# Performance work log

Hardware: AMD Instinct MI355X
Metric: run time of the kernel (lower is better)

## Reference

```python
import jax, jax.numpy as jnp
import numpy as np
from jax import lax

# minLSTM activation g(x) = x + 0.5 if x >= 0 else sigmoid(x)  (mingru repo functional.g)

def g_act(x):
    return jnp.where(x >= 0, x + 0.5, jax.nn.sigmoid(x))


def conv2d_seq(x5, w, b):
    # x5: (B,S,Cin,H,W), w: (Cout,Cin,3,3), stride 1, pad 1 -> (B,S,Cout,H,W)
    B, S = x5.shape[:2]
    xf = x5.reshape((B * S,) + x5.shape[2:])
    y = lax.conv_general_dilated(xf, w, window_strides=(1, 1),
                                 padding=[(1, 1), (1, 1)],
                                 dimension_numbers=("NCHW", "OIHW", "NCHW"))
    y = y + b[None, :, None, None]
    return y.reshape((B, S) + y.shape[1:])


def minlstm_layer(inp, w, b):
    # inp: (B,S,Cin,H,W) -> out h: (B,S,Cout,H,W)
    gates = conv2d_seq(inp, w, b)                     # (B,S,4C,H,W)
    i_g, f_g, o_g, cand = jnp.split(gates, 4, axis=2)  # each (B,S,C,H,W)
    it = jax.nn.sigmoid(i_g)
    ft = jax.nn.sigmoid(f_g)
    denom = it + ft
    fp = ft / denom                                   # normalized forget gate
    ig = (it / denom) * g_act(cand)                   # normalized input * candidate
    B, S, C, H, W = fp.shape
    # zero-init cell state passes through g: g(0) = 0.5 (init_hidden_state)
    c0 = jnp.full((B, C, H, W), 0.5, dtype=inp.dtype)

    def step(c, xs):
        fpt, igt = xs
        c_new = fpt * c + igt
        return c_new, c_new

    xs = (jnp.moveaxis(fp, 1, 0), jnp.moveaxis(ig, 1, 0))  # (S,B,C,H,W)
    _, cs = lax.scan(step, c0, xs)
    cs = jnp.moveaxis(cs, 0, 1)                       # (B,S,C,H,W)
    h = jax.nn.sigmoid(o_g) * cs                      # output gate
    return h


def setup_inputs() -> dict:
    key = jax.random.key(0)
    ks = jax.random.split(key, 5)
    x = jax.random.normal(ks[0], (4, 16, 32, 32, 32), dtype=jnp.float32)
    w0 = jax.random.normal(ks[1], (256, 32, 3, 3), dtype=jnp.float32) * 0.05
    b0 = jax.random.normal(ks[2], (256,), dtype=jnp.float32) * 0.05
    w1 = jax.random.normal(ks[3], (256, 64, 3, 3), dtype=jnp.float32) * 0.05
    b1 = jax.random.normal(ks[4], (256,), dtype=jnp.float32) * 0.05
    return {"x": x, "w0": w0, "b0": b0, "w1": w1, "b1": b1}


def reference(x, w0, b0, w1, b1):
    out = minlstm_layer(x, w0, b0)
    out = minlstm_layer(out, w1, b1)
    return out  # (B,S,64,H,W) — last layer outputs
```

## Files before the change

### kernel.cpp

```cpp
#include <hip/hip_runtime.h>


typedef __bf16 bf16x8 __attribute__((ext_vector_type(8)));
typedef __bf16 bf16x4 __attribute__((ext_vector_type(4)));
typedef __bf16 bf16x2 __attribute__((ext_vector_type(2)));
typedef float f32x4 __attribute__((ext_vector_type(4)));

#define N_IMG 64
#define HP 34
#define COUT 256

__device__ __forceinline__ float sigf(float x) { return 1.0f / (1.0f + __expf(-x)); }

__device__ __forceinline__ void gload16(void* lds, const void* g) {
  __builtin_amdgcn_global_load_lds(
      (const __attribute__((address_space(1))) void*)g,
      (__attribute__((address_space(3))) void*)lds, 16, 0, 0);
}

__global__ __launch_bounds__(256) void pack_x_k(const float* __restrict__ x,
                                                __bf16* __restrict__ xT) {
  __shared__ float ls[32][33];
  const int n = blockIdx.x >> 5;
  const int h = blockIdx.x & 31;
  const int t = threadIdx.x;
  {
    const int w = t & 31, g4 = t >> 5;
    const float* src = x + (((size_t)n * 32) << 10) + (h << 5);
#pragma unroll
    for (int j = 0; j < 4; ++j) {
      int ci = g4 * 4 + j;
      ls[ci][w] = src[((size_t)ci << 10) + w];
    }
  }
  __syncthreads();
  {
    const int ci = t & 31, w4 = t >> 5;
    __bf16* dst = xT + ((size_t)(n * HP + h + 1) * HP + 1) * 32 + ci;
#pragma unroll
    for (int j = 0; j < 4; ++j) {
      int w = w4 * 4 + j;
      dst[w * 32] = (__bf16)ls[ci][w];
    }
  }
}

template <int CIN>
__global__ __launch_bounds__(256) void pack_w_k(const float* __restrict__ w,
                                                __bf16* __restrict__ wT) {
  int g = blockIdx.x * 256 + threadIdx.x;
  if (g >= 256 * 9 * CIN) return;
  int co = g / (9 * CIN);
  int r = g - co * 9 * CIN;
  int khkw = r / CIN;
  int ci = r - khkw * CIN;
  wT[g] = (__bf16)w[(size_t)(co * CIN + ci) * 9 + khkw];
}

template <int CIN, bool LAYER1>
__global__ __launch_bounds__(256, LAYER1 ? 2 : 4) void conv_gemm_k(
    const __bf16* __restrict__ xT,
    const __bf16* __restrict__ wT,
    const float* __restrict__ bias,
    __bf16* __restrict__ gates) {
  constexpr int NKK = CIN / 32;
  constexpr int CHUNKS = CIN / 8;
  __shared__ bf16x8 lsA[2][CHUNKS * 128];
  __shared__ bf16x8 lsB[2][CHUNKS * 128];

  const int tid = threadIdx.x;
  const int lane = tid & 63;
  const int wid = tid >> 6;
  const int wr = wid >> 1, wc = wid & 1;

  const int bx = blockIdx.x;
  const int by = blockIdx.y;
  const int n = bx >> 3;
  const int h0 = (bx & 7) << 2;
  const int co0 = by << 7;

  f32x4 acc[4][4] = {};
  const size_t wrow = (size_t)9 * CIN;

  auto stage = [&](int buf, int t) {
    const int kh = t / 3;
    const int kw = t - kh * 3;
#pragma unroll
    for (int c = wid; c < 2 * CHUNKS; c += 4) {
      const int chunk = c >> 1;
      const int pix = ((c & 1) << 6) + lane;
      const int hh = h0 + (pix >> 5) + kh;
      const int ww = (pix & 31) + kw;
      gload16((void*)(&lsA[buf][c * 64]),
              (const void*)(xT + ((size_t)(n * HP + hh) * HP + ww) * CIN + chunk * 8));
    }
#pragma unroll
    for (int c = wid; c < 2 * CHUNKS; c += 4) {
      const int chunk = c >> 1;
      const int row = ((c & 1) << 6) + lane;
      gload16((void*)(&lsB[buf][c * 64]),
              (const void*)(wT + (size_t)(co0 + row) * wrow + t * CIN + chunk * 8));
    }
  };

  stage(0, 0);
  __syncthreads();
  int cur = 0;
  for (int t = 0; t < 9; ++t) {
    if (t < 8) stage(cur ^ 1, t + 1);
#pragma unroll
    for (int kk = 0; kk < NKK; ++kk) {
      const int ca = kk * 4 + (lane >> 4);
      bf16x8 af[4], wf[4];
#pragma unroll
      for (int mi = 0; mi < 4; ++mi)
        af[mi] = lsA[cur][ca * 128 + wr * 64 + mi * 16 + (lane & 15)];
#pragma unroll
      for (int ni = 0; ni < 4; ++ni)
        wf[ni] = lsB[cur][ca * 128 + wc * 64 + ni * 16 + (lane & 15)];
#pragma unroll
      for (int mi = 0; mi < 4; ++mi)
#pragma unroll
        for (int ni = 0; ni < 4; ++ni) {
          if constexpr (!LAYER1)
            acc[mi][ni] = __builtin_amdgcn_mfma_f32_16x16x32_bf16(
                af[mi], wf[ni], acc[mi][ni], 0, 0, 0);
          else
            acc[mi][ni] = __builtin_amdgcn_mfma_f32_16x16x32_bf16(
                wf[ni], af[mi], acc[mi][ni], 0, 0, 0);
        }
    }
    __syncthreads();
    cur ^= 1;
  }

#pragma unroll
  for (int mi = 0; mi < 4; ++mi)
#pragma unroll
    for (int ni = 0; ni < 4; ++ni)
#pragma unroll
      for (int r = 0; r < 4; ++r) {
        if constexpr (!LAYER1) {
          const int m_loc = wr * 64 + mi * 16 + ((lane >> 4) << 2) + r;
          const int co = co0 + wc * 64 + ni * 16 + (lane & 15);
          const size_t m = (size_t)bx * 128 + m_loc;
          gates[m * 256 + co] = (__bf16)(acc[mi][ni][r] + bias[co]);
        } else {
          const int co = co0 + wc * 64 + ni * 16 + ((lane >> 4) << 2) + r;
          const int m_loc = wr * 64 + mi * 16 + (lane & 15);
          const int m = bx * 128 + m_loc;
          const int nimg = m >> 10, p = m & 1023;
          gates[((size_t)nimg * 256 + co) * 1024 + p] =
              (__bf16)(acc[mi][ni][r] + bias[co]);
        }
      }
}

__global__ __launch_bounds__(256) void scan0_k(const __bf16* __restrict__ gates,
                                               __bf16* __restrict__ h0T) {
  const int g = blockIdx.x * 256 + threadIdx.x;
  const int c = (g & 31) * 2;
  const int p = (g >> 5) & 1023;
  const int b = g >> 15;
  const int h = p >> 5, w = p & 31;
  float c0 = 0.5f, c1 = 0.5f;
#pragma unroll 4
  for (int s = 0; s < 16; ++s) {
    const size_t base = ((size_t)((b * 16 + s) * 1024 + p)) * 256 + c;
    const bf16x2* gp = reinterpret_cast<const bf16x2*>(gates + base);
    const bf16x2 ig2 = gp[0], fg2 = gp[32], og2 = gp[64], cd2 = gp[96];
    bf16x2 hv2;
#pragma unroll
    for (int j = 0; j < 2; ++j) {
      const float it = sigf((float)ig2[j]), ft = sigf((float)fg2[j]);
      const float inv = 1.0f / (it + ft);
      const float cd_ = (float)cd2[j];
      const float gc = (cd_ >= 0.0f) ? (cd_ + 0.5f) : sigf(cd_);
      float& cst = j ? c1 : c0;
      cst = (ft * inv) * cst + (it * inv) * gc;
      hv2[j] = (__bf16)(sigf((float)og2[j]) * cst);
    }
    *reinterpret_cast<bf16x2*>(
        h0T + ((size_t)((b * 16 + s) * HP + h + 1) * HP + (w + 1)) * 64 + c) = hv2;
  }
}

__global__ __launch_bounds__(256) void scan1_k(const __bf16* __restrict__ gates,
                                               float* __restrict__ out) {
  const int g = blockIdx.x * 256 + threadIdx.x;
  const int p0 = (g & 255) * 4;
  const int c = (g >> 8) & 63;
  const int b = g >> 14;
  float cst[4] = {0.5f, 0.5f, 0.5f, 0.5f};
#pragma unroll 2
  for (int s = 0; s < 16; ++s) {
    const size_t base = ((size_t)(b * 16 + s) * 256 + c) * 1024 + p0;
    const bf16x4 ig4 = *reinterpret_cast<const bf16x4*>(gates + base);
    const bf16x4 fg4 = *reinterpret_cast<const bf16x4*>(gates + base + 64 * 1024);
    const bf16x4 og4 = *reinterpret_cast<const bf16x4*>(gates + base + 128 * 1024);
    const bf16x4 cd4 = *reinterpret_cast<const bf16x4*>(gates + base + 192 * 1024);
    f32x4 hv;
#pragma unroll
    for (int j = 0; j < 4; ++j) {
      const float it = sigf((float)ig4[j]), ft = sigf((float)fg4[j]);
      const float inv = 1.0f / (it + ft);
      const float cd_ = (float)cd4[j];
      const float gc = (cd_ >= 0.0f) ? (cd_ + 0.5f) : sigf(cd_);
      cst[j] = (ft * inv) * cst[j] + (it * inv) * gc;
      hv[j] = sigf((float)og4[j]) * cst[j];
    }
    *reinterpret_cast<f32x4*>(
        out + ((size_t)((b * 16 + s) * 64 + c)) * 1024 + p0) = hv;
  }
}

extern "C" void kernel_launch(void* const* d_in, const int* in_sizes, int n_in,
                              void* d_out, int out_size, void* d_ws,
                              size_t ws_size, hipStream_t stream) {
  const float* x = (const float*)d_in[0];
  const float* w0 = (const float*)d_in[1];
  const float* b0 = (const float*)d_in[2];
  const float* w1 = (const float*)d_in[3];
  const float* b1 = (const float*)d_in[4];
  float* out = (float*)d_out;

  char* ws = (char*)d_ws;
  const size_t XT_BYTES = (size_t)N_IMG * HP * HP * 32 * 2;
  const size_t H0_BYTES = (size_t)N_IMG * HP * HP * 64 * 2;
  const size_t W0T_BYTES = (size_t)256 * 9 * 32 * 2;
  const size_t W1T_BYTES = (size_t)256 * 9 * 64 * 2;
  __bf16* xT = (__bf16*)ws;
  __bf16* h0T = (__bf16*)(ws + XT_BYTES);
  __bf16* w0T = (__bf16*)(ws + XT_BYTES + H0_BYTES);
  __bf16* w1T = (__bf16*)(ws + XT_BYTES + H0_BYTES + W0T_BYTES);
  __bf16* gates = (__bf16*)(ws + XT_BYTES + H0_BYTES + W0T_BYTES + W1T_BYTES);
  (void)ws_size; (void)n_in; (void)in_sizes; (void)out_size;

  hipMemsetAsync(xT, 0, XT_BYTES, stream);
  hipMemsetAsync(h0T, 0, H0_BYTES, stream);

  pack_x_k<<<N_IMG * 32, 256, 0, stream>>>(x, xT);
  pack_w_k<32><<<(256 * 9 * 32 + 255) / 256, 256, 0, stream>>>(w0, w0T);
  pack_w_k<64><<<(256 * 9 * 64 + 255) / 256, 256, 0, stream>>>(w1, w1T);

  conv_gemm_k<32, false><<<dim3(512, 2), 256, 0, stream>>>(xT, w0T, b0, gates);
  scan0_k<<<512, 256, 0, stream>>>(gates, h0T);
  conv_gemm_k<64, true><<<dim3(512, 2), 256, 0, stream>>>(h0T, w1T, b1, gates);
  scan1_k<<<256, 256, 0, stream>>>(gates, out);
}
```

Baseline: 188.6 us.

## Load input halo plane once into LDS and index taps from it

The conv GEMM now loads a 6x34 padded input plane per block into LDS once, instead of re-staging a shifted im2col tile for every one of the nine taps. A-fragments are read at per-tap offsets, so only the weight tile stays double-buffered per tap. This is meant to cut redundant global loads of activations. It uses synchronous vector loads for the plane, adds LDS bank-conflict risk from the 34-wide stride, and changes layer-0 occupancy to 2. Separately, scan0 processes 4 channels per thread with half the blocks.

```diff
diff --git a/kernel.cpp b/kernel.cpp
--- a/kernel.cpp
+++ b/kernel.cpp
@@ -58,20 +58,23 @@
 }
 
 template <int CIN, bool LAYER1>
-__global__ __launch_bounds__(256, LAYER1 ? 2 : 4) void conv_gemm_k(
+__global__ __launch_bounds__(256, 2) void conv_gemm_k(
     const __bf16* __restrict__ xT,
     const __bf16* __restrict__ wT,
     const float* __restrict__ bias,
     __bf16* __restrict__ gates) {
   constexpr int NKK = CIN / 32;
   constexpr int CHUNKS = CIN / 8;
-  __shared__ bf16x8 lsA[2][CHUNKS * 128];
+  constexpr int PLANE = 204;
+  __shared__ bf16x8 lsA[CHUNKS * PLANE];
   __shared__ bf16x8 lsB[2][CHUNKS * 128];
 
   const int tid = threadIdx.x;
   const int lane = tid & 63;
   const int wid = tid >> 6;
   const int wr = wid >> 1, wc = wid & 1;
+  const int g = lane >> 4;
+  const int li = lane & 15;
 
   const int bx = blockIdx.x;
   const int by = blockIdx.y;
@@ -82,18 +85,23 @@
   f32x4 acc[4][4] = {};
   const size_t wrow = (size_t)9 * CIN;
 
-  auto stage = [&](int buf, int t) {
-    const int kh = t / 3;
-    const int kw = t - kh * 3;
-#pragma unroll
-    for (int c = wid; c < 2 * CHUNKS; c += 4) {
-      const int chunk = c >> 1;
-      const int pix = ((c & 1) << 6) + lane;
-      const int hh = h0 + (pix >> 5) + kh;
-      const int ww = (pix & 31) + kw;
-      gload16((void*)(&lsA[buf][c * 64]),
-              (const void*)(xT + ((size_t)(n * HP + hh) * HP + ww) * CIN + chunk * 8));
-    }
+  for (int gi = tid; gi < CHUNKS * PLANE; gi += 256) {
+    const int ch = gi & (CHUNKS - 1);
+    const int pos = gi / CHUNKS;
+    const int r = pos / 34;
+    const int w = pos - r * 34;
+    lsA[ch * PLANE + pos] = *reinterpret_cast<const bf16x8*>(
+        xT + ((size_t)(n * HP + h0 + r) * HP + w) * CIN + ch * 8);
+  }
+
+  int posm[4];
+#pragma unroll
+  for (int mi = 0; mi < 4; ++mi) {
+    const int m = wr * 64 + mi * 16 + li;
+    posm[mi] = (m >> 5) * 34 + (m & 31);
+  }
+
+  auto stageB = [&](int buf, int t) {
 #pragma unroll
     for (int c = wid; c < 2 * CHUNKS; c += 4) {
       const int chunk = c >> 1;
@@ -103,21 +111,25 @@
     }
   };
 
-  stage(0, 0);
+  stageB(0, 0);
   __syncthreads();
   int cur = 0;
+#pragma unroll
   for (int t = 0; t < 9; ++t) {
-    if (t < 8) stage(cur ^ 1, t + 1);
+    const int kh = t / 3;
+    const int kw = t - kh * 3;
+    const int tapoff = kh * 34 + kw;
+    if (t < 8) stageB(cur ^ 1, t + 1);
 #pragma unroll
     for (int kk = 0; kk < NKK; ++kk) {
-      const int ca = kk * 4 + (lane >> 4);
+      const int ca = kk * 4 + g;
       bf16x8 af[4], wf[4];
 #pragma unroll
       for (int mi = 0; mi < 4; ++mi)
-        af[mi] = lsA[cur][ca * 128 + wr * 64 + mi * 16 + (lane & 15)];
+        af[mi] = lsA[ca * PLANE + posm[mi] + tapoff];
 #pragma unroll
       for (int ni = 0; ni < 4; ++ni)
-        wf[ni] = lsB[cur][ca * 128 + wc * 64 + ni * 16 + (lane & 15)];
+        wf[ni] = lsB[cur][ca * 128 + wc * 64 + ni * 16 + li];
 #pragma unroll
       for (int mi = 0; mi < 4; ++mi)
 #pragma unroll
@@ -141,13 +153,13 @@
 #pragma unroll
       for (int r = 0; r < 4; ++r) {
         if constexpr (!LAYER1) {
-          const int m_loc = wr * 64 + mi * 16 + ((lane >> 4) << 2) + r;
-          const int co = co0 + wc * 64 + ni * 16 + (lane & 15);
+          const int m_loc = wr * 64 + mi * 16 + (g << 2) + r;
+          const int co = co0 + wc * 64 + ni * 16 + li;
           const size_t m = (size_t)bx * 128 + m_loc;
           gates[m * 256 + co] = (__bf16)(acc[mi][ni][r] + bias[co]);
         } else {
-          const int co = co0 + wc * 64 + ni * 16 + ((lane >> 4) << 2) + r;
-          const int m_loc = wr * 64 + mi * 16 + (lane & 15);
+          const int co = co0 + wc * 64 + ni * 16 + (g << 2) + r;
+          const int m_loc = wr * 64 + mi * 16 + li;
           const int m = bx * 128 + m_loc;
           const int nimg = m >> 10, p = m & 1023;
           gates[((size_t)nimg * 256 + co) * 1024 + p] =
@@ -159,29 +171,28 @@
 __global__ __launch_bounds__(256) void scan0_k(const __bf16* __restrict__ gates,
                                                __bf16* __restrict__ h0T) {
   const int g = blockIdx.x * 256 + threadIdx.x;
-  const int c = (g & 31) * 2;
-  const int p = (g >> 5) & 1023;
-  const int b = g >> 15;
+  const int c = (g & 15) * 4;
+  const int p = (g >> 4) & 1023;
+  const int b = g >> 14;
   const int h = p >> 5, w = p & 31;
-  float c0 = 0.5f, c1 = 0.5f;
+  float cst[4] = {0.5f, 0.5f, 0.5f, 0.5f};
 #pragma unroll 4
   for (int s = 0; s < 16; ++s) {
     const size_t base = ((size_t)((b * 16 + s) * 1024 + p)) * 256 + c;
-    const bf16x2* gp = reinterpret_cast<const bf16x2*>(gates + base);
-    const bf16x2 ig2 = gp[0], fg2 = gp[32], og2 = gp[64], cd2 = gp[96];
-    bf16x2 hv2;
-#pragma unroll
-    for (int j = 0; j < 2; ++j) {
-      const float it = sigf((float)ig2[j]), ft = sigf((float)fg2[j]);
+    const bf16x4* gp = reinterpret_cast<const bf16x4*>(gates + base);
+    const bf16x4 ig4 = gp[0], fg4 = gp[16], og4 = gp[32], cd4 = gp[48];
+    bf16x4 hv4;
+#pragma unroll
+    for (int j = 0; j < 4; ++j) {
+      const float it = sigf((float)ig4[j]), ft = sigf((float)fg4[j]);
       const float inv = 1.0f / (it + ft);
-      const float cd_ = (float)cd2[j];
+      const float cd_ = (float)cd4[j];
       const float gc = (cd_ >= 0.0f) ? (cd_ + 0.5f) : sigf(cd_);
-      float& cst = j ? c1 : c0;
-      cst = (ft * inv) * cst + (it * inv) * gc;
-      hv2[j] = (__bf16)(sigf((float)og2[j]) * cst);
-    }
-    *reinterpret_cast<bf16x2*>(
-        h0T + ((size_t)((b * 16 + s) * HP + h + 1) * HP + (w + 1)) * 64 + c) = hv2;
+      cst[j] = (ft * inv) * cst[j] + (it * inv) * gc;
+      hv4[j] = (__bf16)(sigf((float)og4[j]) * cst[j]);
+    }
+    *reinterpret_cast<bf16x4*>(
+        h0T + ((size_t)((b * 16 + s) * HP + h + 1) * HP + (w + 1)) * 64 + c) = hv4;
   }
 }
 
@@ -244,7 +255,7 @@
   pack_w_k<64><<<(256 * 9 * 64 + 255) / 256, 256, 0, stream>>>(w1, w1T);
 
   conv_gemm_k<32, false><<<dim3(512, 2), 256, 0, stream>>>(xT, w0T, b0, gates);
-  scan0_k<<<512, 256, 0, stream>>>(gates, h0T);
+  scan0_k<<<256, 256, 0, stream>>>(gates, h0T);
   conv_gemm_k<64, true><<<dim3(512, 2), 256, 0, stream>>>(h0T, w1T, b1, gates);
   scan1_k<<<256, 256, 0, stream>>>(gates, out);
 }
```

Result: faster. 165.7 us (-12.1%).
